# Kernel tuning notes

Hardware: AMD Instinct MI355X
Metric: run time of the kernel (lower is better)

## Reference

```python
import jax, jax.numpy as jnp
import numpy as np

EMBED = 384
HEADS = 12
DH = EMBED // HEADS  # 32, lucidrains default dim_heads = dim // heads
EPS = 1e-5


def _layernorm(t, g, b):
    mu = jnp.mean(t, axis=-1, keepdims=True)
    var = jnp.mean(jnp.square(t - mu), axis=-1, keepdims=True)
    return (t - mu) * jax.lax.rsqrt(var + EPS) * g + b


def _self_attn(t2, Wq, Wkv, Wo, bo):
    # t2: (N, T, D) -> multi-head self attention (lucidrains SelfAttention)
    N, T, D = t2.shape
    q = t2 @ Wq
    k, v = jnp.split(t2 @ Wkv, 2, axis=-1)
    def split_heads(z):
        return z.reshape(N, T, HEADS, DH).transpose(0, 2, 1, 3)  # (N,H,T,DH)
    q, k, v = map(split_heads, (q, k, v))
    dots = jnp.einsum('nhie,nhje->nhij', q, k) * (DH ** -0.5)
    o = jnp.einsum('nhij,nhje->nhie', jax.nn.softmax(dots, axis=-1), v)
    o = o.transpose(0, 2, 1, 3).reshape(N, T, D)
    return o @ Wo + bo


def _axial(xcl, axis, Wq, Wkv, Wo, bo):
    # xcl channels-last: (b, 3, 16, 16, C); attend along `axis` (1, 2 or 3)
    y = jnp.moveaxis(xcl, axis, -2)
    sh = y.shape
    o = _self_attn(y.reshape(-1, sh[-2], sh[-1]), Wq, Wkv, Wo, bo)
    return jnp.moveaxis(o.reshape(sh), -2, axis)


def setup_inputs() -> dict:
    key = jax.random.key(0)
    ks = jax.random.split(key, 24)
    d, mlp = EMBED, 4 * EMBED
    s = 0.02
    inp = {'x': jax.random.normal(ks[0], (128, 384, 3, 16, 16), jnp.float32)}
    for i in range(3):  # one SelfAttention per axial dim (slice, h, w)
        inp[f'Wq{i}'] = (jax.random.normal(ks[1 + 3 * i], (d, d)) * s).astype(jnp.float32)
        inp[f'Wkv{i}'] = (jax.random.normal(ks[2 + 3 * i], (d, 2 * d)) * s).astype(jnp.float32)
        inp[f'Wo{i}'] = (jax.random.normal(ks[3 + 3 * i], (d, d)) * s).astype(jnp.float32)
        inp[f'bo{i}'] = jnp.zeros((d,), jnp.float32)
    inp['g1'] = jnp.ones((d,), jnp.float32)
    inp['be1'] = jnp.zeros((d,), jnp.float32)
    inp['W1m'] = (jax.random.normal(ks[10], (d, mlp)) * s).astype(jnp.float32)
    inp['b1m'] = jnp.zeros((mlp,), jnp.float32)
    inp['W2m'] = (jax.random.normal(ks[11], (mlp, d)) * s).astype(jnp.float32)
    inp['b2m'] = jnp.zeros((d,), jnp.float32)
    inp['g2'] = jnp.ones((d,), jnp.float32)
    inp['be2'] = jnp.zeros((d,), jnp.float32)
    return inp


def reference(x, Wq0, Wkv0, Wo0, bo0, Wq1, Wkv1, Wo1, bo1, Wq2, Wkv2, Wo2, bo2,
              g1, be1, W1m, b1m, W2m, b2m, g2, be2):
    # x: (B, C=384, 3, 16, 16); dropout is identity in eval mode
    xcl = jnp.moveaxis(x, 1, -1)  # (B, 3, 16, 16, C)
    attn = (_axial(xcl, 1, Wq0, Wkv0, Wo0, bo0)
            + _axial(xcl, 2, Wq1, Wkv1, Wo1, bo1)
            + _axial(xcl, 3, Wq2, Wkv2, Wo2, bo2))  # sum_axial_out=True
    xcl = xcl + attn  # residual
    B = xcl.shape[0]
    t = xcl.reshape(B, 3 * 16 * 16, EMBED)  # == x.flatten(2).transpose(1,2)
    t = _layernorm(t, g1, be1)
    m = jax.nn.gelu(t @ W1m + b1m, approximate=False) @ W2m + b2m
    t = _layernorm(t + m, g2, be2)
    return jnp.moveaxis(t.reshape(B, 3, 16, 16, EMBED), -1, 1)
```

## Files before the change

### kernel.cpp

```cpp
#include <hip/hip_runtime.h>

typedef unsigned short u16;
typedef __bf16 bf16;
typedef bf16  bf16x4 __attribute__((ext_vector_type(4)));
typedef bf16  bf16x8 __attribute__((ext_vector_type(8)));
typedef float f32x4  __attribute__((ext_vector_type(4)));

__device__ __forceinline__ u16  f2b(float v) { return __builtin_bit_cast(u16, (bf16)v); }
__device__ __forceinline__ float b2f(u16 b)  { return (float)__builtin_bit_cast(bf16, b); }

__global__ void probe_dtype(const float* xf, int* flag) {
    __shared__ int cnt[256];
    const int tid = threadIdx.x;
    int good = 0;
#pragma unroll
    for (int i = 0; i < 4; ++i) {
        const float a = fabsf(xf[tid * 4 + i]);
        if (a > 9.5e-7f && a < 1.0e6f) good++;
    }
    cnt[tid] = good;
    __syncthreads();
    if (tid == 0) { int s = 0; for (int i = 0; i < 256; ++i) s += cnt[i]; *flag = (s > 512) ? 1 : 0; }
}

__device__ __forceinline__ float rd_flag(const void* p, int i, int f32) {
    return f32 ? ((const float*)p)[i] : b2f(((const u16*)p)[i]);
}

__global__ __launch_bounds__(256)
void cvt_all(const void* bo0, const void* bo1, const void* bo2,
             const void* g1, const void* be1, const void* g2, const void* be2,
             const void* b1m, const void* b2m, bf16* vp, const int* flag)
{
    const int f32 = *flag;
    const int i = blockIdx.x * 256 + threadIdx.x;
    if (i < 384) {
        vp[i] = (bf16)(rd_flag(bo0, i, f32) + rd_flag(bo1, i, f32) + rd_flag(bo2, i, f32));
    } else if (i < 768)  { vp[i] = (bf16)rd_flag(g1,  i - 384,  f32); }
    else if (i < 1152)   { vp[i] = (bf16)rd_flag(be1, i - 768,  f32); }
    else if (i < 1536)   { vp[i] = (bf16)rd_flag(g2,  i - 1152, f32); }
    else if (i < 1920)   { vp[i] = (bf16)rd_flag(be2, i - 1536, f32); }
    else if (i < 3456)   { vp[i] = (bf16)rd_flag(b1m, i - 1920, f32); }
    else                 { vp[i] = (bf16)rd_flag(b2m, i - 3456, f32); }
}

struct SrcPtrs { const void* p[11]; };
__global__ __launch_bounds__(256)
void wtrans_all(SrcPtrs srcs, u16* wsbase, const int* flag)
{
    const int prefix[12] = {0, 144, 432, 576, 720, 1008, 1152, 1296, 1584, 1728, 2304, 2880};
    const int Carr[11]   = {384, 768, 384,  384, 768, 384,  384, 768, 384,  1536, 384};
    const int OSarr[11]  = {384, 384, 1152, 384, 384, 1152, 384, 384, 1152, 384, 1536};
    const int DOarr[11]  = {0, 147456, 1327104, 442368, 589824, 1327488,
                            884736, 1032192, 1327872, 1769472, 2359296};

    __shared__ u16 tile[32][34];
    const int f32 = *flag;
    const int bid = blockIdx.x;
    int s = 0;
#pragma unroll
    for (int k = 0; k < 11; ++k) if (bid >= prefix[k + 1]) s = k + 1;
    const int tix = bid - prefix[s];
    const int C = Carr[s], ostride = OSarr[s];
    const int tilesX = C >> 5;
    const int c0 = (tix % tilesX) * 32, r0 = (tix / tilesX) * 32;
    const void* in = srcs.p[s];
    u16* out = wsbase + DOarr[s];

    const int tx = threadIdx.x & 31, ty = threadIdx.x >> 5;
#pragma unroll
    for (int i = 0; i < 4; ++i) {
        const int idx = (r0 + ty + i * 8) * C + c0 + tx;
        tile[ty + i * 8][tx] = f32 ? f2b(((const float*)in)[idx]) : ((const u16*)in)[idx];
    }
    __syncthreads();
#pragma unroll
    for (int i = 0; i < 4; ++i)
        out[(size_t)(c0 + ty + i * 8) * ostride + r0 + tx] = tile[tx][ty + i * 8];
}

__global__ void transpose_cvt(const void* in, u16* out, size_t base_off, int R, int C, int ostride, const int* flag) {
    __shared__ u16 tile[32][34];
    const int f32 = *flag;
    const int c0 = blockIdx.x * 32, r0 = blockIdx.y * 32;
    const size_t bi = base_off + (size_t)blockIdx.z * R * C;
    const size_t bo = (size_t)blockIdx.z * C * ostride;
    const int tx = threadIdx.x, ty = threadIdx.y;
#pragma unroll
    for (int i = 0; i < 4; ++i) {
        const size_t idx = bi + (size_t)(r0 + ty + i * 8) * C + c0 + tx;
        tile[ty + i * 8][tx] = f32 ? f2b(((const float*)in)[idx]) : ((const u16*)in)[idx];
    }
    __syncthreads();
#pragma unroll
    for (int i = 0; i < 4; ++i)
        out[bo + (size_t)(c0 + ty + i * 8) * ostride + r0 + tx] = tile[tx][ty + i * 8];
}

__device__ __forceinline__ void gld_lds16(const bf16* g, bf16* l) {
    __builtin_amdgcn_global_load_lds((__attribute__((address_space(1))) void*)g,
                                     (__attribute__((address_space(3))) void*)l,
                                     16, 0, 0);
}

template<int MODE>
__global__ __launch_bounds__(512)
void gemm256(const bf16* __restrict__ A, const bf16* __restrict__ BT,
             bf16* C, const bf16* __restrict__ bias, int M, int N, int K)
{
    __shared__ __align__(16) bf16 sm[65536];
    const int tid = threadIdx.x;

    const int gx = gridDim.x, gy = gridDim.y;
    int lin = blockIdx.y * gx + blockIdx.x;
    const int nwg = gx * gy;
    const int q = nwg >> 3, r8 = nwg & 7;
    const int xcd = lin & 7, idx = lin >> 3;
    lin = (xcd < r8 ? xcd * (q + 1) : r8 * (q + 1) + (xcd - r8) * q) + idx;
    const int bm0 = (lin / gy) * 256;
    const int bn0 = (lin % gy) * 256;

    const int lane = tid & 63, wid = tid >> 6;
    const int wr = wid >> 2, wc = wid & 3;
    const int fr = lane & 15, fg = lane >> 4;
    const int arow = tid >> 3;
    const int scol = ((tid & 7) ^ (arow & 7)) << 3;

    const bf16* Ab = A  + (size_t)(bm0 + arow) * K + scol;
    const bf16* Bb = BT + (size_t)(bn0 + arow) * K + scol;

    bf16* const lA0 = sm;
    bf16* const lA1 = sm + 16384;
    bf16* const lB0 = sm + 32768;
    bf16* const lB1 = sm + 49152;

    f32x4 acc[8][4] = {};
    const int NT = K >> 6;

#pragma unroll
    for (int i = 0; i < 4; ++i) gld_lds16(Ab + (size_t)i * 64 * K, lA0 + i * 4096 + tid * 8);
#pragma unroll
    for (int i = 0; i < 4; ++i) gld_lds16(Bb + (size_t)i * 64 * K, lB0 + i * 4096 + tid * 8);
    __syncthreads();

    const int sw = fr & 7;
    for (int t = 0; t < NT; ++t) {
        if (t + 1 < NT) {
            const int k0 = (t + 1) << 6;
            bf16* la = ((t + 1) & 1) ? lA1 : lA0;
            bf16* lb = ((t + 1) & 1) ? lB1 : lB0;
#pragma unroll
            for (int i = 0; i < 4; ++i) gld_lds16(Ab + k0 + (size_t)i * 64 * K, la + i * 4096 + tid * 8);
#pragma unroll
            for (int i = 0; i < 4; ++i) gld_lds16(Bb + k0 + (size_t)i * 64 * K, lb + i * 4096 + tid * 8);
        }
        const bf16* la = (t & 1) ? lA1 : lA0;
        const bf16* lb = (t & 1) ? lB1 : lB0;
#pragma unroll
        for (int kk = 0; kk < 2; ++kk) {
            const int so = ((((kk << 2) + fg) ^ sw) << 3);
            bf16x8 bfv[4];
#pragma unroll
            for (int n = 0; n < 4; ++n)
                bfv[n] = *(const bf16x8*)&lb[(wc * 64 + n * 16 + fr) * 64 + so];
#pragma unroll
            for (int m = 0; m < 8; ++m) {
                const bf16x8 af = *(const bf16x8*)&la[(wr * 128 + m * 16 + fr) * 64 + so];
#pragma unroll
                for (int n = 0; n < 4; ++n)
                    acc[m][n] = __builtin_amdgcn_mfma_f32_16x16x32_bf16(af, bfv[n], acc[m][n], 0, 0, 0);
            }
        }
        __syncthreads();
    }

#pragma unroll
    for (int n = 0; n < 4; ++n) {
        const int col = wc * 64 + n * 16 + fr;
        const float bv = (MODE == 2) ? (float)bias[bn0 + col] : 0.f;
#pragma unroll
        for (int m = 0; m < 8; ++m) {
            const int row0 = wr * 128 + m * 16 + fg * 4;
#pragma unroll
            for (int r = 0; r < 4; ++r) {
                float v = acc[m][n][r];
                if (MODE == 2) { v += bv; v = 0.5f * v * (1.f + erff(v * 0.70710678118654752f)); }
                sm[(row0 + r) * 256 + col] = (bf16)v;
            }
        }
    }
    __syncthreads();
#pragma unroll
    for (int it = 0; it < 16; ++it) {
        const int chunk = it * 512 + tid;
        const int row = chunk >> 5, c8 = (chunk & 31) << 3;
        *(bf16x8*)&C[(size_t)(bm0 + row) * N + bn0 + c8] = *(const bf16x8*)&sm[row * 256 + c8];
    }
}

template<int MODE>
__global__ __launch_bounds__(256)
void gemm_bt(const bf16* __restrict__ A, const bf16* __restrict__ BT,
             bf16* C, const bf16* __restrict__ bias,
             const bf16* add, int M, int N, int K)
{
    __shared__ __align__(16) bf16 sm[16384];
    const int tid = threadIdx.x;

    const int gx = gridDim.x, gy = gridDim.y;
    int lin = blockIdx.y * gx + blockIdx.x;
    const int nwg = gx * gy;
    const int q = nwg >> 3, r8 = nwg & 7;
    const int xcd = lin & 7, idx = lin >> 3;
    lin = (xcd < r8 ? xcd * (q + 1) : r8 * (q + 1) + (xcd - r8) * q) + idx;
    const int bm0 = (lin / gy) * 128;
    const int bn0 = (lin % gy) * 128;

    const int lane = tid & 63, wid = tid >> 6;
    const int wr = wid >> 1, wc = wid & 1;
    const int fr = lane & 15, fg = lane >> 4;
    const int arow = tid >> 3;
    const int scol = ((tid & 7) ^ (arow & 7)) << 3;

    const bf16* Ab = A  + (size_t)(bm0 + arow) * K + scol;
    const bf16* Bb = BT + (size_t)(bn0 + arow) * K + scol;

    bf16* const lA = sm;
    bf16* const lB = sm + 8192;

    f32x4 acc[4][4] = {};
    const int NT = K >> 6;
    const int sw = fr & 7;

    for (int t = 0; t < NT; ++t) {
        __syncthreads();
        const int k0 = t << 6;
#pragma unroll
        for (int i = 0; i < 4; ++i) gld_lds16(Ab + k0 + (size_t)i * 32 * K, lA + i * 2048 + tid * 8);
#pragma unroll
        for (int i = 0; i < 4; ++i) gld_lds16(Bb + k0 + (size_t)i * 32 * K, lB + i * 2048 + tid * 8);
        __syncthreads();
#pragma unroll
        for (int kk = 0; kk < 2; ++kk) {
            bf16x8 af[4], bfv[4];
#pragma unroll
            for (int m = 0; m < 4; ++m)
                af[m] = *(const bf16x8*)&lA[(wr * 64 + m * 16 + fr) * 64 + ((((kk << 2) + fg) ^ sw) << 3)];
#pragma unroll
            for (int n = 0; n < 4; ++n)
                bfv[n] = *(const bf16x8*)&lB[(wc * 64 + n * 16 + fr) * 64 + ((((kk << 2) + fg) ^ sw) << 3)];
#pragma unroll
            for (int m = 0; m < 4; ++m)
#pragma unroll
                for (int n = 0; n < 4; ++n)
                    acc[m][n] = __builtin_amdgcn_mfma_f32_16x16x32_bf16(af[m], bfv[n], acc[m][n], 0, 0, 0);
        }
    }
    __syncthreads();

    float* lc = (float*)sm;
#pragma unroll
    for (int half = 0; half < 2; ++half) {
        if (wr == half) {
#pragma unroll
            for (int n = 0; n < 4; ++n) {
                const int col = wc * 64 + n * 16 + fr;
#pragma unroll
                for (int m = 0; m < 4; ++m)
#pragma unroll
                    for (int r2 = 0; r2 < 4; ++r2)
                        lc[(m * 16 + fg * 4 + r2) * 128 + col] = acc[m][n][r2];
            }
        }
        __syncthreads();
#pragma unroll
        for (int i = 0; i < 8; ++i) {
            const int chunk = i * 256 + tid;
            const int row = chunk >> 5, cb = (chunk & 31) * 4;
            const size_t goff = (size_t)(bm0 + half * 64 + row) * N + bn0 + cb;
            const f32x4 v = ((const f32x4*)lc)[chunk];
            bf16x4 o;
            if (MODE == 1) {
                const bf16x4 bv = *(const bf16x4*)&bias[bn0 + cb];
                const bf16x4 av = *(const bf16x4*)&add[goff];
#pragma unroll
                for (int e = 0; e < 4; ++e) o[e] = (bf16)(v[e] + (float)bv[e] + (float)av[e]);
            } else {
#pragma unroll
                for (int e = 0; e < 4; ++e) o[e] = (bf16)v[e];
            }
            *(bf16x4*)&C[goff] = o;
        }
        __syncthreads();
    }
}

__global__ __launch_bounds__(768)
void attn16_lds(const bf16* __restrict__ QKV, bf16* __restrict__ O, int tstride, int lastmul, int qs, int os)
{
    __shared__ bf16 kv[16 * 1160];
    const int tid  = threadIdx.x;
    const int lane = tid & 63, h = tid >> 6;
    const int seq  = blockIdx.x;
    const int b    = seq / 48, r2 = seq % 48;
    const int s    = r2 >> 4, last = r2 & 15;
    const int tbase = b * 768 + s * 256 + last * lastmul;
    const int fr = lane & 15, fg = lane >> 4;

#pragma unroll
    for (int k = 0; k < 3; ++k) {
        const int c = k * 768 + tid;
        const int row = c / 144, col = (c % 144) * 8;
        *(bf16x8*)&kv[row * 1160 + col] =
            *(const bf16x8*)&QKV[(size_t)(tbase + row * tstride) * qs + col];
    }
    __syncthreads();

    const bf16* base = kv + h * 32;
    const bf16x8 qf = *(const bf16x8*)&base[fr * 1160 + fg * 8];
    const bf16x8 kf = *(const bf16x8*)&base[fr * 1160 + 384 + fg * 8];
    const f32x4 z = {0.f, 0.f, 0.f, 0.f};
    f32x4 S = __builtin_amdgcn_mfma_f32_16x16x32_bf16(kf, qf, z, 0, 0, 0);

    const float sc = 0.17677669529663687f;
    float mx = fmaxf(fmaxf(S[0], S[1]), fmaxf(S[2], S[3]));
    mx = fmaxf(mx, __shfl_xor(mx, 16));
    mx = fmaxf(mx, __shfl_xor(mx, 32));
    float p[4], sum = 0.f;
#pragma unroll
    for (int r = 0; r < 4; ++r) { p[r] = __expf((S[r] - mx) * sc); sum += p[r]; }
    sum += __shfl_xor(sum, 16);
    sum += __shfl_xor(sum, 32);
    const float inv = 1.f / sum;

    bf16x8 pa;
#pragma unroll
    for (int j = 0; j < 8; ++j) {
        const int srcg = 2 * fg + (j >> 2);
        const float v = __shfl(p[j & 3], fr + 16 * (srcg & 3));
        pa[j] = (bf16)(fg < 2 ? v * inv : 0.f);
    }

#pragma unroll
    for (int t = 0; t < 2; ++t) {
        bf16x8 vf;
#pragma unroll
        for (int j = 0; j < 8; ++j) {
            const int key = fg * 8 + j;
            vf[j] = (fg < 2) ? base[key * 1160 + 768 + fr + 16 * t] : (bf16)0.f;
        }
        f32x4 o = __builtin_amdgcn_mfma_f32_16x16x32_bf16(pa, vf, z, 0, 0, 0);
#pragma unroll
        for (int r = 0; r < 4; ++r)
            O[(size_t)(tbase + (fg * 4 + r) * tstride) * os + h * 32 + fr + 16 * t] = (bf16)o[r];
    }
}

__global__ __launch_bounds__(256)
void attn3(const bf16* __restrict__ QKV, bf16* __restrict__ O, int qs, int os)
{
    const int t    = blockIdx.x * 256 + threadIdx.x;
    const int head = t % 12;
    const int seq  = t / 12;
    const int b    = seq >> 8, hw = seq & 255;
    const size_t base  = (size_t)(b * 768 + hw) * qs + head * 32;
    const size_t tstep = (size_t)256 * qs;

    float s[3][3] = {};
#pragma unroll
    for (int c = 0; c < 4; ++c) {
        bf16x8 q[3], k[3];
#pragma unroll
        for (int i = 0; i < 3; ++i) {
            q[i] = *(const bf16x8*)(QKV + base + i * tstep + c * 8);
            k[i] = *(const bf16x8*)(QKV + base + i * tstep + 384 + c * 8);
        }
#pragma unroll
        for (int i = 0; i < 3; ++i)
#pragma unroll
            for (int j = 0; j < 3; ++j) {
                float a = 0.f;
#pragma unroll
                for (int e = 0; e < 8; ++e) a += (float)q[i][e] * (float)k[j][e];
                s[i][j] += a;
            }
    }
    const float sc = 0.17677669529663687f;
    float p[3][3];
#pragma unroll
    for (int i = 0; i < 3; ++i) {
        const float mx = fmaxf(s[i][0], fmaxf(s[i][1], s[i][2]));
        float sum = 0.f;
#pragma unroll
        for (int j = 0; j < 3; ++j) { p[i][j] = __expf((s[i][j] - mx) * sc); sum += p[i][j]; }
        const float inv = 1.f / sum;
#pragma unroll
        for (int j = 0; j < 3; ++j) p[i][j] *= inv;
    }
    const size_t obase = (size_t)(b * 768 + hw) * os + head * 32;
#pragma unroll
    for (int c = 0; c < 4; ++c) {
        bf16x8 v[3];
#pragma unroll
        for (int j = 0; j < 3; ++j) v[j] = *(const bf16x8*)(QKV + base + j * tstep + 768 + c * 8);
#pragma unroll
        for (int i = 0; i < 3; ++i) {
            bf16x8 ov;
#pragma unroll
            for (int e = 0; e < 8; ++e)
                ov[e] = (bf16)(p[i][0] * (float)v[0][e] + p[i][1] * (float)v[1][e] + p[i][2] * (float)v[2][e]);
            *(bf16x8*)(O + obase + (size_t)i * 256 * os + c * 8) = ov;
        }
    }
}

__global__ __launch_bounds__(256)
void ln_kernel(const bf16* __restrict__ in, bf16* __restrict__ out,
               const bf16* __restrict__ g, const bf16* __restrict__ be, int ntok)
{
    const int w    = (blockIdx.x * 256 + threadIdx.x) >> 6;
    const int lane = threadIdx.x & 63;
    if (w >= ntok) return;
    const bf16* row = in + (size_t)w * 384;
    float x[6], sum = 0.f;
#pragma unroll
    for (int i = 0; i < 6; ++i) { x[i] = (float)row[lane + i * 64]; sum += x[i]; }
#pragma unroll
    for (int o = 32; o >= 1; o >>= 1) sum += __shfl_xor(sum, o);
    const float mu = sum * (1.f / 384.f);
    float vs = 0.f;
#pragma unroll
    for (int i = 0; i < 6; ++i) { const float d = x[i] - mu; vs += d * d; }
#pragma unroll
    for (int o = 32; o >= 1; o >>= 1) vs += __shfl_xor(vs, o);
    const float rstd = rsqrtf(vs * (1.f / 384.f) + 1e-5f);
    bf16* orow = out + (size_t)w * 384;
#pragma unroll
    for (int i = 0; i < 6; ++i)
        orow[lane + i * 64] = (bf16)((x[i] - mu) * rstd * (float)g[lane + i * 64] + (float)be[lane + i * 64]);
}

__global__ __launch_bounds__(256)
void ln_transpose_out(const bf16* __restrict__ in, void* out, size_t base_off,
                      const bf16* __restrict__ g, const bf16* __restrict__ be, const int* flag)
{
    __shared__ bf16 tile[32][388];
    const int f32 = *flag;
    const int tid = threadIdx.x;
    const int lane = tid & 63, w = tid >> 6;
    const int r0 = blockIdx.x * 32;
    const int zz = blockIdx.y;
    const bf16* inz = in + ((size_t)zz * 768 + r0) * 384;

#pragma unroll
    for (int p = 0; p < 8; ++p) {
        const int tok = p * 4 + w;
        const bf16* row = inz + (size_t)tok * 384;
        float x[6], sum = 0.f;
#pragma unroll
        for (int i = 0; i < 6; ++i) { x[i] = (float)row[lane + i * 64]; sum += x[i]; }
#pragma unroll
        for (int o = 32; o >= 1; o >>= 1) sum += __shfl_xor(sum, o);
        const float mu = sum * (1.f / 384.f);
        float vs = 0.f;
#pragma unroll
        for (int i = 0; i < 6; ++i) { const float d = x[i] - mu; vs += d * d; }
#pragma unroll
        for (int o = 32; o >= 1; o >>= 1) vs += __shfl_xor(vs, o);
        const float rstd = rsqrtf(vs * (1.f / 384.f) + 1e-5f);
#pragma unroll
        for (int i = 0; i < 6; ++i)
            tile[tok][lane + i * 64] =
                (bf16)((x[i] - mu) * rstd * (float)g[lane + i * 64] + (float)be[lane + i * 64]);
    }
    __syncthreads();

    const size_t bo = base_off + (size_t)zz * 384 * 768;
#pragma unroll
    for (int it = 0; it < 48; ++it) {
        const int idx = it * 256 + tid;
        const int c = idx >> 5, r = idx & 31;
        const u16 v = __builtin_bit_cast(u16, tile[r][c]);
        const size_t o = bo + (size_t)c * 768 + r0 + r;
        if (f32) ((float*)out)[o] = b2f(v); else ((u16*)out)[o] = v;
    }
}

extern "C" void kernel_launch(void* const* d_in, const int* in_sizes, int n_in,
                              void* d_out, int out_size, void* d_ws, size_t ws_size,
                              hipStream_t stream)
{
    const void* x = d_in[0];
    const void *Wq[3], *Wkv[3], *Wo[3], *bo[3];
    for (int i = 0; i < 3; ++i) {
        Wq[i]  = d_in[1 + 4 * i];
        Wkv[i] = d_in[2 + 4 * i];
        Wo[i]  = d_in[3 + 4 * i];
        bo[i]  = d_in[4 + 4 * i];
    }
    const void* g1  = d_in[13];
    const void* be1 = d_in[14];
    const void* W1m = d_in[15];
    const void* b1m = d_in[16];
    const void* W2m = d_in[17];
    const void* b2m = d_in[18];
    const void* g2  = d_in[19];
    const void* be2 = d_in[20];

    char* ws = (char*)d_ws;
    bf16* qkvT = (bf16*)(ws);
    bf16* woTf = (bf16*)(ws + 2654208ull);
    bf16* w1mT = (bf16*)(ws + 3538944ull);
    bf16* w2mT = (bf16*)(ws + 4718592ull);
    bf16* vp   = (bf16*)(ws + 5898240ull);
    bf16* vboS = vp;
    bf16* vg1  = vp + 384;  bf16* vbe1 = vp + 768;
    bf16* vg2  = vp + 1152; bf16* vbe2 = vp + 1536;
    bf16* vb1m = vp + 1920; bf16* vb2m = vp + 3456;
    int* dflag = (int*)(ws + 5909504ull);
    const size_t WB = 6553600ull;

    int NB = 32;
    while (NB > 2) {
        size_t need = WB + (size_t)NB * 768 * (3 * 384 + 2 * 1152 + 1536) * 2;
        if (need <= ws_size) break;
        NB >>= 1;
    }
    const int Tc = NB * 768;
    const size_t tokB = (size_t)Tc * 384 * 2;
    bf16* Xc    = (bf16*)(ws + WB);
    bf16* ABc   = (bf16*)(ws + WB + tokB);
    bf16* T1c   = (bf16*)(ws + WB + 2 * tokB);
    bf16* ATOc  = (bf16*)(ws + WB + 3 * tokB);
    bf16* QKVc  = (bf16*)(ws + WB + 6 * tokB);
    bf16* BIGc  = (bf16*)(ws + WB + 9 * tokB);

    probe_dtype<<<1, 256, 0, stream>>>((const float*)x, dflag);
    cvt_all<<<15, 256, 0, stream>>>(bo[0], bo[1], bo[2], g1, be1, g2, be2, b1m, b2m, vp, dflag);
    SrcPtrs sp;
    sp.p[0] = Wq[0]; sp.p[1] = Wkv[0]; sp.p[2] = Wo[0];
    sp.p[3] = Wq[1]; sp.p[4] = Wkv[1]; sp.p[5] = Wo[1];
    sp.p[6] = Wq[2]; sp.p[7] = Wkv[2]; sp.p[8] = Wo[2];
    sp.p[9] = W1m;   sp.p[10] = W2m;
    wtrans_all<<<2880, 256, 0, stream>>>(sp, (u16*)ws, dflag);

    const dim3 tb(32, 8);
    for (int b0 = 0; b0 < 128; b0 += NB) {
        const size_t xoff = (size_t)b0 * 384 * 768;
        transpose_cvt<<<dim3(24, 12, NB), tb, 0, stream>>>(x, (u16*)Xc, xoff, 384, 768, 384, dflag);

        for (int i = 0; i < 3; ++i) {
            gemm_bt<0><<<dim3(Tc / 128, 9), 256, 0, stream>>>(Xc, qkvT + (size_t)(i * 1152) * 384,
                                                              QKVc, nullptr, nullptr, Tc, 1152, 384);
            if (i == 0)      attn3     <<<NB * 12, 256, 0, stream>>>(QKVc, ATOc,              1152, 1152);
            else if (i == 1) attn16_lds<<<NB * 48, 768, 0, stream>>>(QKVc, ATOc + 384, 16, 1, 1152, 1152);
            else             attn16_lds<<<NB * 48, 768, 0, stream>>>(QKVc, ATOc + 768, 1, 16, 1152, 1152);
        }

        gemm_bt<1><<<dim3(Tc / 128, 3), 256, 0, stream>>>(ATOc, woTf, ABc, vboS, Xc, Tc, 384, 1152);

        ln_kernel<<<Tc / 4, 256, 0, stream>>>(ABc, T1c, vg1, vbe1, Tc);
        gemm256<2><<<dim3(Tc / 256, 6), 512, 0, stream>>>(T1c, w1mT, BIGc, vb1m, Tc, 1536, 384);
        gemm_bt<1><<<dim3(Tc / 128, 3), 256, 0, stream>>>(BIGc, w2mT, ABc, vb2m, T1c, Tc, 384, 1536);
        ln_transpose_out<<<dim3(24, NB), 256, 0, stream>>>(ABc, d_out, xoff, vg2, vbe2, dflag);
    }
}
```

Before: 1.428 ms.

## Batch three axial QKV GEMMs and merge two attention launches via grid z/y

The three per-axis QKV projection GEMMs become one launch using blockIdx.z, with per-axis pointer offsets into a triple-sized QKV buffer. The two 16-length axial attentions are merged into one kernel that picks its axis from blockIdx.y. This cuts kernel launches and gives larger grids that fill the GPU better. The cost is three times the QKV workspace, which may shrink the chunk size NB when workspace is tight.

After: 1.403 ms, median of 2. No clear change (-1.7%).

```diff
diff --git a/kernel.cpp b/kernel.cpp
--- a/kernel.cpp
+++ b/kernel.cpp
@@ -202,7 +202,8 @@
 __global__ __launch_bounds__(256)
 void gemm_bt(const bf16* __restrict__ A, const bf16* __restrict__ BT,
              bf16* C, const bf16* __restrict__ bias,
-             const bf16* add, int M, int N, int K)
+             const bf16* add, int M, int N, int K,
+             size_t zA, size_t zB, size_t zC)
 {
     __shared__ __align__(16) bf16 sm[16384];
     const int tid = threadIdx.x;
@@ -215,6 +216,10 @@
     lin = (xcd < r8 ? xcd * (q + 1) : r8 * (q + 1) + (xcd - r8) * q) + idx;
     const int bm0 = (lin / gy) * 128;
     const int bn0 = (lin % gy) * 128;
+
+    A  += (size_t)blockIdx.z * zA;
+    BT += (size_t)blockIdx.z * zB;
+    C  += (size_t)blockIdx.z * zC;
 
     const int lane = tid & 63, wid = tid >> 6;
     const int wr = wid >> 1, wc = wid & 1;
@@ -296,9 +301,15 @@
 }
 
 __global__ __launch_bounds__(768)
-void attn16_lds(const bf16* __restrict__ QKV, bf16* __restrict__ O, int tstride, int lastmul, int qs, int os)
+void attn16_lds2(const bf16* __restrict__ QKV3, bf16* __restrict__ O, size_t qkvz, int qs, int os)
 {
     __shared__ bf16 kv[16 * 1160];
+    const int axis = blockIdx.y;
+    const int tstride = axis ? 1 : 16;
+    const int lastmul = axis ? 16 : 1;
+    const bf16* QKV = QKV3 + (size_t)(axis + 1) * qkvz;
+    bf16* Oc = O + 384 * (axis + 1);
+
     const int tid  = threadIdx.x;
     const int lane = tid & 63, h = tid >> 6;
     const int seq  = blockIdx.x;
@@ -352,7 +363,7 @@
         f32x4 o = __builtin_amdgcn_mfma_f32_16x16x32_bf16(pa, vf, z, 0, 0, 0);
 #pragma unroll
         for (int r = 0; r < 4; ++r)
-            O[(size_t)(tbase + (fg * 4 + r) * tstride) * os + h * 32 + fr + 16 * t] = (bf16)o[r];
+            Oc[(size_t)(tbase + (fg * 4 + r) * tstride) * os + h * 32 + fr + 16 * t] = (bf16)o[r];
     }
 }
 
@@ -522,7 +533,7 @@
 
     int NB = 32;
     while (NB > 2) {
-        size_t need = WB + (size_t)NB * 768 * (3 * 384 + 2 * 1152 + 1536) * 2;
+        size_t need = WB + (size_t)NB * 768 * (3 * 384 + 4 * 1152 + 1536) * 2;
         if (need <= ws_size) break;
         NB >>= 1;
     }
@@ -532,8 +543,9 @@
     bf16* ABc   = (bf16*)(ws + WB + tokB);
     bf16* T1c   = (bf16*)(ws + WB + 2 * tokB);
     bf16* ATOc  = (bf16*)(ws + WB + 3 * tokB);
-    bf16* QKVc  = (bf16*)(ws + WB + 6 * tokB);
-    bf16* BIGc  = (bf16*)(ws + WB + 9 * tokB);
+    bf16* QKV3c = (bf16*)(ws + WB + 6 * tokB);
+    bf16* BIGc  = (bf16*)(ws + WB + 15 * tokB);
+    const size_t qkvz = (size_t)Tc * 1152;
 
     probe_dtype<<<1, 256, 0, stream>>>((const float*)x, dflag);
     cvt_all<<<15, 256, 0, stream>>>(bo[0], bo[1], bo[2], g1, be1, g2, be2, b1m, b2m, vp, dflag);
@@ -549,19 +561,18 @@
         const size_t xoff = (size_t)b0 * 384 * 768;
         transpose_cvt<<<dim3(24, 12, NB), tb, 0, stream>>>(x, (u16*)Xc, xoff, 384, 768, 384, dflag);
 
-        for (int i = 0; i < 3; ++i) {
-            gemm_bt<0><<<dim3(Tc / 128, 9), 256, 0, stream>>>(Xc, qkvT + (size_t)(i * 1152) * 384,
-                                                              QKVc, nullptr, nullptr, Tc, 1152, 384);
-            if (i == 0)      attn3     <<<NB * 12, 256, 0, stream>>>(QKVc, ATOc,              1152, 1152);
-            else if (i == 1) attn16_lds<<<NB * 48, 768, 0, stream>>>(QKVc, ATOc + 384, 16, 1, 1152, 1152);
-            else             attn16_lds<<<NB * 48, 768, 0, stream>>>(QKVc, ATOc + 768, 1, 16, 1152, 1152);
-        }
-
-        gemm_bt<1><<<dim3(Tc / 128, 3), 256, 0, stream>>>(ATOc, woTf, ABc, vboS, Xc, Tc, 384, 1152);
+        gemm_bt<0><<<dim3(Tc / 128, 9, 3), 256, 0, stream>>>(
+            Xc, qkvT, QKV3c, nullptr, nullptr, Tc, 1152, 384,
+            0, (size_t)1152 * 384, qkvz);
+
+        attn3<<<NB * 12, 256, 0, stream>>>(QKV3c, ATOc, 1152, 1152);
+        attn16_lds2<<<dim3(NB * 48, 2), 768, 0, stream>>>(QKV3c, ATOc, qkvz, 1152, 1152);
+
+        gemm_bt<1><<<dim3(Tc / 128, 3), 256, 0, stream>>>(ATOc, woTf, ABc, vboS, Xc, Tc, 384, 1152, 0, 0, 0);
 
         ln_kernel<<<Tc / 4, 256, 0, stream>>>(ABc, T1c, vg1, vbe1, Tc);
         gemm256<2><<<dim3(Tc / 256, 6), 512, 0, stream>>>(T1c, w1mT, BIGc, vb1m, Tc, 1536, 384);
-        gemm_bt<1><<<dim3(Tc / 128, 3), 256, 0, stream>>>(BIGc, w2mT, ABc, vb2m, T1c, Tc, 384, 1536);
+        gemm_bt<1><<<dim3(Tc / 128, 3), 256, 0, stream>>>(BIGc, w2mT, ABc, vb2m, T1c, Tc, 384, 1536, 0, 0, 0);
         ln_transpose_out<<<dim3(24, NB), 256, 0, stream>>>(ABc, d_out, xoff, vg2, vbe2, dflag);
     }
 }
```
